# Performance work log

Measured on AMD Instinct MI355X. Metric: run time of the kernel, lower is better.

Reference implementation:

```python
import jax, jax.numpy as jnp
import numpy as np

H, D, J, T, IN = 8, 32, 22, 6, 256   # heads, head_dim, joint_num, time_len-2, input_dim
S = 3 * J                            # sequence axis of attention (66)
NEG = -9e15


def _domain_mask():
    m = np.ones((S, S), np.float32)
    m[0:J, 2 * J:3 * J] = 0.0
    m[2 * J:3 * J, 0:J] = 0.0
    return jnp.asarray(m)


def setup_inputs() -> dict:
    key = jax.random.key(0)
    ks = jax.random.split(key, 5)
    s = 0.02
    return {
        "x": jax.random.normal(ks[0], (512, T, S, IN), jnp.float32),
        "Wq": jax.random.normal(ks[1], (H * D, IN), jnp.float32) * s,
        "bq": jnp.zeros((H * D,), jnp.float32),
        "Wk": jax.random.normal(ks[2], (H * D, IN), jnp.float32) * s,
        "bk": jnp.zeros((H * D,), jnp.float32),
        "Wv": jax.random.normal(ks[3], (H * D, IN), jnp.float32) * s,
        "bv": jnp.zeros((H * D,), jnp.float32),
        "Wc": jax.random.normal(ks[4], (J, S), jnp.float32) * s,
        "bc": jnp.zeros((J,), jnp.float32),
    }


def reference(x, Wq, bq, Wk, bk, Wv, bv, Wc, bc):
    B = x.shape[0]
    mask = _domain_mask()

    def proj(W, b):
        # (B,T,S,IN) @ (IN,H*D) -> (B,T,S,H,D) -> (B,T,H,S,D)
        return (x @ W.T + b).reshape(B, T, S, H, D).transpose(0, 1, 3, 2, 4)

    q = proj(Wq, bq)
    k = proj(Wk, bk)
    v = jax.nn.relu(proj(Wv, bv))

    scores = jnp.einsum('bthqd,bthkd->bthqk', q, k) / jnp.sqrt(jnp.float32(D))
    scores = scores * mask
    # joint_num == 22 branch: threshold-based pruning against row max
    m = jnp.max(scores, axis=-1, keepdims=True)
    scores = jnp.where(jnp.abs(scores) <= m / 9.0, NEG, scores)
    attn = jax.nn.softmax(scores, axis=-1)

    out = jnp.einsum('bthqk,bthkd->bthqd', attn, v)          # (B,T,H,S,D)
    # cls Linear over the S axis: (B,T,H,D,S) -> (B,T,H,D,J), then back to (B,T,H,J,D)
    out = jnp.einsum('bthsd,js->bthjd', out, Wc) + bc[None, None, None, :, None]
    out = out.transpose(0, 1, 3, 2, 4)                        # (B,T,J,H,D)
    return out.reshape(B, T * J, H * D)
```

## Files before the change

kernel.cpp:

```cpp
#include <hip/hip_runtime.h>
#include <hip/hip_bf16.h>


constexpr int T  = 6;
constexpr int S  = 66;
constexpr int IN = 256;
constexpr int H  = 8;
constexpr int D  = 32;
constexpr int J  = 22;
constexpr float NEG = -9e15f;
constexpr float INV_SQRT_D = 0.17677669529663688110f;

#define XM2H_OFF 16384
#define XM2L_OFF 20480
#define W_OFF    24576
#define W_LO     12288
#define QH_OFF   0
#define QL_OFF   4752
#define KH_OFF   9504
#define KL_OFF   14256
#define VTH_OFF  28512
#define VTL_OFF  35168
#define INV_OFF  41824
#define AOT_OFF  42096
#define PH_OFF   0
#define PL_OFF   14256
#define P_STRIDE 216
#define WCH_OFF  28512
#define WCL_OFF  35168
#define SMEM_BYTES 49152

#define WSW_STRIDE 24576
#define WSWC_OFF   786432
#define WS_W       799744ull
#define XIMG_OFF   799744
#define XIMG_BT    65536
#define WS_FULL    (799744ull + 3072ull * 65536ull)

typedef float f32x4   __attribute__((ext_vector_type(4)));
typedef float f32x16  __attribute__((ext_vector_type(16)));
typedef short bf16x8  __attribute__((ext_vector_type(8)));
typedef short s4v     __attribute__((ext_vector_type(4)));

__device__ __forceinline__ unsigned cvtpk(float a, float b) {
    unsigned r;
    asm("v_cvt_pk_bf16_f32 %0, %1, %2" : "=v"(r) : "v"(a), "v"(b));
    return r;
}
__device__ __forceinline__ float bfh2f(unsigned short h) {
    return __uint_as_float(((unsigned)h) << 16);
}
__device__ __forceinline__ void split2(float a, float b, unsigned& hi, unsigned& lo) {
    unsigned h = cvtpk(a, b);
    float ra = a - __uint_as_float(h << 16);
    float rb = b - __uint_as_float(h & 0xffff0000u);
    lo = cvtpk(ra, rb);
    hi = h;
}
__device__ __forceinline__ bf16x8 ld_bf16x8_a8(const short* p) {
    s4v a = *(const s4v*)p;
    s4v b = *(const s4v*)(p + 4);
    return __builtin_shufflevector(a, b, 0, 1, 2, 3, 4, 5, 6, 7);
}
__device__ __forceinline__ void gload16(const void* g, void* l) {
    __builtin_amdgcn_global_load_lds(
        (const __attribute__((address_space(1))) unsigned*)g,
        (__attribute__((address_space(3))) unsigned*)l, 16, 0, 0);
}

__global__ __launch_bounds__(256)
void presplit_all(const float* __restrict__ Wq, const float* __restrict__ Wk,
                  const float* __restrict__ Wv, const float* __restrict__ Wc,
                  const float* __restrict__ x, unsigned char* __restrict__ ws)
{
    __shared__ __align__(16) unsigned char lds[16384];
    const int tid = threadIdx.x;
    if (blockIdx.x < 199) {
        int gid = blockIdx.x * 256 + tid;
        if (gid < 49152) {
            int img = gid / 1536, u = gid - img * 1536;
            int row = u >> 4, c = u & 15, k0 = c << 2;
            int mat = row >> 5, dd = row & 31;
            int chunk = img & 3, hh = img >> 2;
            const float* Wm = (mat == 0) ? Wq : (mat == 1) ? Wk : Wv;
            float4 v = *(const float4*)(Wm + (size_t)(hh * 32 + dd) * IN + chunk * 64 + c * 4);
            uint2 hi, lo;
            split2(v.x, v.y, hi.x, lo.x);
            split2(v.z, v.w, hi.y, lo.y);
            int tile  = (mat << 2) + (k0 >> 4);
            int lanei = dd + (((k0 >> 3) & 1) << 5);
            int byte  = (tile << 10) + (lanei << 4) + ((k0 & 7) << 1);
            unsigned char* base = ws + (size_t)img * WSW_STRIDE;
            *(uint2*)(base + byte)        = hi;
            *(uint2*)(base + W_LO + byte) = lo;
        } else if (gid < 49152 + 1664) {
            int g2  = gid - 49152;
            int row = g2 / 52, cu = g2 - row * 52;
            int c0  = 2 * cu;
            float a = (row < 22 && c0     < 66) ? Wc[row * 66 + c0]     : 0.f;
            float b = (row < 22 && c0 + 1 < 66) ? Wc[row * 66 + c0 + 1] : 0.f;
            unsigned hi, lo;
            split2(a, b, hi, lo);
            *(unsigned*)(ws + WSWC_OFF + row * 208 + 4 * cu)        = hi;
            *(unsigned*)(ws + WSWC_OFF + 6656 + row * 208 + 4 * cu) = lo;
        }
    } else {
        const int bid = blockIdx.x - 199;
        const int chunk = bid & 3;
        const int bt = bid >> 2;
        const float* xg = x + (size_t)bt * S * IN + chunk * 64;
        for (int u = tid; u < 1024; u += 256) {
            int s = u >> 4, c = u & 15;
            int rel = ((s << 7) + (c << 3)) ^ ((s & 7) << 4);
            float4 v = *(const float4*)(xg + (size_t)s * IN + c * 4);
            uint2 hi, lo;
            split2(v.x, v.y, hi.x, lo.x);
            split2(v.z, v.w, hi.y, lo.y);
            *(uint2*)(lds + rel)        = hi;
            *(uint2*)(lds + 8192 + rel) = lo;
        }
        __syncthreads();
        const int lane = tid & 63, wid = tid >> 6;
        unsigned char* img = ws + XIMG_OFF + (size_t)bt * XIMG_BT + chunk * 16384;
        for (int i = wid; i < 16; i += 4) {
            int comp = (i >= 8) ? 1 : 0;
            int ti = i - comp * 8;
            int mtile = ti >> 2, ks = ti & 3;
            int row = mtile * 32 + (lane & 31);
            int rel = ((row << 7) + (ks << 5) + ((lane >> 5) << 4)) ^ ((row & 7) << 4);
            uint4 v = *(const uint4*)(lds + comp * 8192 + rel);
            *(uint4*)(img + (i << 10) + (lane << 4)) = v;
        }
    }
}

template<int MODE>
__global__ __launch_bounds__(256, 3)
void mha_fused_kernel(const float* __restrict__ x,
                      const float* __restrict__ Wq, const float* __restrict__ bq,
                      const float* __restrict__ Wk, const float* __restrict__ bk,
                      const float* __restrict__ Wv, const float* __restrict__ bv,
                      const float* __restrict__ Wc, const float* __restrict__ bc,
                      const unsigned char* __restrict__ ws,
                      float* __restrict__ out)
{
    __shared__ __align__(16) unsigned char smem[SMEM_BYTES];

    const int tid = threadIdx.x;
    const int i0  = blockIdx.x;
    const int h   = (i0 >> 3) & 7;
    const int bt  = (i0 & 7) | ((i0 >> 6) << 3);

    const int wid  = tid >> 6;
    const int lane = tid & 63;
    const int l15  = lane & 15;
    const int quad = lane >> 4;

    for (int u = tid; u < 512; u += 256)
        *(uint4*)(smem + XM2H_OFF + u * 16) = (uint4){0u, 0u, 0u, 0u};

    const f32x16 zacc = {0.f,0.f,0.f,0.f,0.f,0.f,0.f,0.f,0.f,0.f,0.f,0.f,0.f,0.f,0.f,0.f};
    f32x16 accs[3] = {zacc, zacc, zacc};

    const float* xg0 = x + (size_t)bt * S * IN;
    for (int chunk = 0; chunk < 4; ++chunk) {
        __syncthreads();
        const float* xg = xg0 + chunk * 64;
        if constexpr (MODE == 2) {
            const unsigned char* ximg = ws + XIMG_OFF + (size_t)bt * XIMG_BT + chunk * 16384;
            const unsigned char* wimg = ws + (size_t)((h << 2) | chunk) * WSW_STRIDE;
            for (int i = wid; i < 16; i += 4)
                gload16(ximg + (i << 10) + (lane << 4), smem + (i << 10));
            for (int i = wid; i < 24; i += 4)
                gload16(wimg + (i << 10) + (lane << 4), smem + W_OFF + (i << 10));
            if (tid < 32) {
                int s = 64 + (tid >> 4), c = tid & 15;
                float4 v = *(const float4*)(xg + (size_t)s * IN + c * 4);
                uint2 hi, lo;
                split2(v.x, v.y, hi.x, lo.x);
                split2(v.z, v.w, hi.y, lo.y);
                int off = ((c >> 2) << 10) + (((s & 31) + (((c >> 1) & 1) << 5)) << 4)
                        + ((c & 1) << 3);
                *(uint2*)(smem + XM2H_OFF + off) = hi;
                *(uint2*)(smem + XM2L_OFF + off) = lo;
            }
        } else {
            if constexpr (MODE == 1) {
                const unsigned char* wimg = ws + (size_t)((h << 2) | chunk) * WSW_STRIDE;
                for (int i = wid; i < 24; i += 4)
                    gload16(wimg + (i << 10) + (lane << 4), smem + W_OFF + (i << 10));
            } else {
                for (int u = tid; u < 1536; u += 256) {
                    int row = u >> 4, c = u & 15, k0 = c << 2;
                    int mat = row >> 5, dd2 = row & 31;
                    const float* Wm = (mat == 0) ? Wq : (mat == 1) ? Wk : Wv;
                    float4 v = *(const float4*)(Wm + (size_t)(h * 32 + dd2) * IN + chunk * 64 + c * 4);
                    uint2 hi, lo;
                    split2(v.x, v.y, hi.x, lo.x);
                    split2(v.z, v.w, hi.y, lo.y);
                    int tile  = (mat << 2) + (k0 >> 4);
                    int lanei = dd2 + (((k0 >> 3) & 1) << 5);
                    int byte  = (tile << 10) + (lanei << 4) + ((k0 & 7) << 1);
                    *(uint2*)(smem + W_OFF + byte)        = hi;
                    *(uint2*)(smem + W_OFF + W_LO + byte) = lo;
                }
            }
            for (int u = tid; u < 1536; u += 256) {
                int s = u >> 4, c = u & 15, k0 = c << 2;
                if (s >= 66) continue;
                float4 v = *(const float4*)(xg + (size_t)s * IN + c * 4);
                uint2 hi, lo;
                split2(v.x, v.y, hi.x, lo.x);
                split2(v.z, v.w, hi.y, lo.y);
                int ks = k0 >> 4, khalf = (k0 >> 3) & 1, b = (k0 & 7) << 1;
                int off = (ks << 10) + (((s & 31) + (khalf << 5)) << 4) + b;
                if (s < 64) {
                    int base = (s >> 5) * 4096 + off;
                    *(uint2*)(smem + base)        = hi;
                    *(uint2*)(smem + base + 8192) = lo;
                } else {
                    *(uint2*)(smem + XM2H_OFF + off) = hi;
                    *(uint2*)(smem + XM2L_OFF + off) = lo;
                }
            }
        }
        __syncthreads();

        #pragma unroll
        for (int t = 0; t < 3; ++t) {
            int p = wid + 4 * t;
            if (p >= 9) break;
            int mtile = p / 3, mat = p - mtile * 3;
            const unsigned char *xaH, *xaL;
            if (mtile < 2) { xaH = smem + mtile * 4096 + (lane << 4); xaL = xaH + 8192; }
            else           { xaH = smem + XM2H_OFF + (lane << 4);     xaL = xaH + 4096; }
            const unsigned char* wbH = smem + W_OFF + mat * 4096 + (lane << 4);
            #pragma unroll
            for (int ks = 0; ks < 4; ++ks) {
                bf16x8 ah = *(const bf16x8*)(xaH + (ks << 10));
                bf16x8 al = *(const bf16x8*)(xaL + (ks << 10));
                bf16x8 bh = *(const bf16x8*)(wbH + (ks << 10));
                bf16x8 bl = *(const bf16x8*)(wbH + (ks << 10) + W_LO);
                accs[t] = __builtin_amdgcn_mfma_f32_32x32x16_bf16(ah, bh, accs[t], 0, 0, 0);
                accs[t] = __builtin_amdgcn_mfma_f32_32x32x16_bf16(ah, bl, accs[t], 0, 0, 0);
                accs[t] = __builtin_amdgcn_mfma_f32_32x32x16_bf16(al, bh, accs[t], 0, 0, 0);
            }
        }
    }
    __syncthreads();

    {
        short* qh = (short*)(smem + QH_OFF); short* ql = (short*)(smem + QL_OFF);
        short* kh = (short*)(smem + KH_OFF); short* kl = (short*)(smem + KL_OFF);
        const int dd = lane & 31;
        const int half = lane >> 5;
        #pragma unroll
        for (int t = 0; t < 3; ++t) {
            int p = wid + 4 * t;
            if (p >= 9) break;
            int mtile = p / 3, mat = p - mtile * 3;
            const float* bias_p = (mat == 0) ? bq : (mat == 1) ? bk : bv;
            float bias = bias_p[h * 32 + dd];
            if (mat < 2) {
                short* bh_ = (mat == 0) ? qh : kh;
                short* bl_ = (mat == 0) ? ql : kl;
                #pragma unroll
                for (int g = 0; g < 4; ++g) {
                    int sb2 = mtile * 32 + half * 4 + 8 * g;
                    uint2 hi, lo;
                    split2(accs[t][4*g+0] + bias, accs[t][4*g+1] + bias, hi.x, lo.x);
                    split2(accs[t][4*g+2] + bias, accs[t][4*g+3] + bias, hi.y, lo.y);
                    unsigned hs[4] = { hi.x & 0xffffu, hi.x >> 16, hi.y & 0xffffu, hi.y >> 16 };
                    unsigned ls[4] = { lo.x & 0xffffu, lo.x >> 16, lo.y & 0xffffu, lo.y >> 16 };
                    #pragma unroll
                    for (int r = 0; r < 4; ++r) {
                        int s = sb2 + r;
                        if (s < 66) {
                            bh_[s * 36 + dd] = (short)hs[r];
                            bl_[s * 36 + dd] = (short)ls[r];
                        }
                    }
                }
            } else {
                #pragma unroll
                for (int g = 0; g < 4; ++g) {
                    int sb2 = mtile * 32 + half * 4 + 8 * g;
                    float vv[4];
                    #pragma unroll
                    for (int r = 0; r < 4; ++r) {
                        int s = sb2 + r;
                        vv[r] = (s < 66) ? fmaxf(accs[t][4*g+r] + bias, 0.f) : 0.f;
                    }
                    uint2 ph, pl;
                    split2(vv[0], vv[1], ph.x, pl.x);
                    split2(vv[2], vv[3], ph.y, pl.y);
                    *(uint2*)(smem + VTH_OFF + dd * 208 + 2 * sb2) = ph;
                    *(uint2*)(smem + VTL_OFF + dd * 208 + 2 * sb2) = pl;
                }
            }
        }
    }
    __syncthreads();

    {
        const short* qh = (const short*)(smem + QH_OFF);
        const short* ql = (const short*)(smem + QL_OFF);
        const short* kh = (const short*)(smem + KH_OFF);
        const short* kl = (const short*)(smem + KL_OFF);

        auto qk_mfma = [&](int mq, f32x4* acc) {
            int boff = (mq * 16 + l15) * 36 + quad * 8;
            bf16x8 bh = ld_bf16x8_a8(qh + boff);
            bf16x8 bl = ld_bf16x8_a8(ql + boff);
            #pragma unroll
            for (int mk = 0; mk < 5; ++mk) {
                int aoff = (mk * 16 + l15) * 36 + quad * 8;
                bf16x8 ah = ld_bf16x8_a8(kh + aoff);
                bf16x8 al = ld_bf16x8_a8(kl + aoff);
                f32x4 a = (f32x4){0.f, 0.f, 0.f, 0.f};
                a = __builtin_amdgcn_mfma_f32_16x16x32_bf16(ah, bh, a, 0, 0, 0);
                a = __builtin_amdgcn_mfma_f32_16x16x32_bf16(ah, bl, a, 0, 0, 0);
                a = __builtin_amdgcn_mfma_f32_16x16x32_bf16(al, bh, a, 0, 0, 0);
                acc[mk] = a;
            }
        };

        f32x4 accA[5], accB[5];
        qk_mfma(wid, accA);
        if (wid == 3) qk_mfma(4, accB);
        __syncthreads();

        unsigned char* Ph = smem + PH_OFF;
        unsigned char* Pl = smem + PL_OFF;
        float* inv = (float*)(smem + INV_OFF);

        auto sm_store = [&](int mq, f32x4* acc) {
            const int q = mq * 16 + l15;
            float v[5][4];
            #pragma unroll
            for (int mk = 0; mk < 5; ++mk) {
                #pragma unroll
                for (int reg = 0; reg < 4; ++reg) {
                    int k = mk * 16 + quad * 4 + reg;
                    bool invalid = (k >= 66);
                    bool masked = (q < J && k >= 2 * J) || (q >= 2 * J && k < J);
                    float s = acc[mk][reg] * INV_SQRT_D;
                    v[mk][reg] = invalid ? -INFINITY : (masked ? 0.f : s);
                }
            }
            float mm = -INFINITY;
            #pragma unroll
            for (int mk = 0; mk < 5; ++mk)
                #pragma unroll
                for (int reg = 0; reg < 4; ++reg) mm = fmaxf(mm, v[mk][reg]);
            mm = fmaxf(mm, __shfl_xor(mm, 16));
            mm = fmaxf(mm, __shfl_xor(mm, 32));
            const float thr = mm / 9.0f;
            float rm = -INFINITY;
            #pragma unroll
            for (int mk = 0; mk < 5; ++mk) {
                #pragma unroll
                for (int reg = 0; reg < 4; ++reg) {
                    float sv = v[mk][reg];
                    float pr = (fabsf(sv) <= thr) ? NEG : sv;
                    v[mk][reg] = pr;
                    rm = fmaxf(rm, pr);
                }
            }
            rm = fmaxf(rm, __shfl_xor(rm, 16));
            rm = fmaxf(rm, __shfl_xor(rm, 32));
            float e[5][4], lsum = 0.f;
            #pragma unroll
            for (int mk = 0; mk < 5; ++mk) {
                #pragma unroll
                for (int reg = 0; reg < 4; ++reg) {
                    float ev = __expf(v[mk][reg] - rm);
                    e[mk][reg] = ev;
                    lsum += ev;
                }
            }
            lsum += __shfl_xor(lsum, 16);
            lsum += __shfl_xor(lsum, 32);
            if (q < 66) {
                #pragma unroll
                for (int mk = 0; mk < 5; ++mk) {
                    unsigned h0 = cvtpk(e[mk][0], e[mk][1]);
                    unsigned h1 = cvtpk(e[mk][2], e[mk][3]);
                    uint2 hi = {h0, h1}, lo;
                    lo.x = cvtpk(e[mk][0] - bfh2f((unsigned short)h0),
                                 e[mk][1] - bfh2f((unsigned short)(h0 >> 16)));
                    lo.y = cvtpk(e[mk][2] - bfh2f((unsigned short)h1),
                                 e[mk][3] - bfh2f((unsigned short)(h1 >> 16)));
                    int kb = (mk * 16 + quad * 4) * 2;
                    *(uint2*)(Ph + q * P_STRIDE + kb) = hi;
                    *(uint2*)(Pl + q * P_STRIDE + kb) = lo;
                }
                if (quad == 0) inv[q] = 1.0f / lsum;
            }
        };

        sm_store(wid, accA);
        if (wid == 3) sm_store(4, accB);

        for (int u = tid; u < 528; u += 256) {
            int comp = u >= 264 ? 1 : 0, rem = u - comp * 264;
            int row = rem >> 2, slot = rem & 3;
            *(uint2*)(smem + (comp ? PL_OFF : PH_OFF) + row * P_STRIDE + 160 + slot * 8)
                = (uint2){0u, 0u};
        }
    }
    __syncthreads();

    {
        const short* Ph = (const short*)(smem + PH_OFF);
        const short* Pl = (const short*)(smem + PL_OFF);
        const short* vh = (const short*)(smem + VTH_OFF);
        const short* vl = (const short*)(smem + VTL_OFF);
        const float* inv = (const float*)(smem + INV_OFF);
        for (int t = 0; t < 3; ++t) {
            int tt = wid + 4 * t;
            if (tt >= 10) break;
            int mq = tt >> 1, nd = tt & 1;
            f32x4 acc = (f32x4){0.f, 0.f, 0.f, 0.f};
            #pragma unroll
            for (int ks = 0; ks < 3; ++ks) {
                bf16x8 a   = ld_bf16x8_a8(Ph + (mq * 16 + l15) * 108 + ks * 32 + quad * 8);
                bf16x8 al8 = ld_bf16x8_a8(Pl + (mq * 16 + l15) * 108 + ks * 32 + quad * 8);
                bf16x8 b   = *(const bf16x8*)(vh + (nd * 16 + l15) * 104 + ks * 32 + quad * 8);
                bf16x8 bl8 = *(const bf16x8*)(vl + (nd * 16 + l15) * 104 + ks * 32 + quad * 8);
                acc = __builtin_amdgcn_mfma_f32_16x16x32_bf16(a, b, acc, 0, 0, 0);
                acc = __builtin_amdgcn_mfma_f32_16x16x32_bf16(al8, b, acc, 0, 0, 0);
                acc = __builtin_amdgcn_mfma_f32_16x16x32_bf16(a, bl8, acc, 0, 0, 0);
            }
            int dd = nd * 16 + l15, sbase = mq * 16 + quad * 4;
            float o[4];
            #pragma unroll
            for (int reg = 0; reg < 4; ++reg) {
                int qs = sbase + reg;
                o[reg] = (qs < 66) ? acc[reg] * inv[qs] : 0.f;
            }
            uint2 pk;
            pk.x = cvtpk(o[0], o[1]);
            pk.y = cvtpk(o[2], o[3]);
            *(uint2*)(smem + AOT_OFF + dd * 208 + 2 * sbase) = pk;
        }
        for (int u = tid; u < 384; u += 256) {
            int row = u / 12, kcol = 80 + 2 * (u % 12);
            *(unsigned*)(smem + AOT_OFF + row * 208 + 2 * kcol) = 0u;
        }
    }
    __syncthreads();

    if constexpr (MODE >= 1) {
        const unsigned char* wc = ws + WSWC_OFF;
        for (int i = wid; i < 13; i += 4)
            gload16(wc + (i << 10) + (lane << 4), smem + WCH_OFF + (i << 10));
    } else {
        for (int u = tid; u < 726; u += 256) {
            int row = u / 33, cp = u - row * 33;
            float2 w = *(const float2*)(Wc + row * 66 + 2 * cp);
            unsigned hi, lo;
            split2(w.x, w.y, hi, lo);
            *(unsigned*)(smem + WCH_OFF + row * 208 + 4 * cp) = hi;
            *(unsigned*)(smem + WCL_OFF + row * 208 + 4 * cp) = lo;
        }
        for (int u = tid; u < 836; u += 256) {
            int comp = u >= 418 ? 1 : 0, rem = comp ? u - 418 : u;
            int row = rem / 19, kcol = 66 + 2 * (rem % 19);
            *(unsigned*)(smem + (comp ? WCL_OFF : WCH_OFF) + row * 208 + 2 * kcol) = 0u;
        }
    }
    __syncthreads();

    {
        const short* Wch = (const short*)(smem + WCH_OFF);
        const short* Wcl = (const short*)(smem + WCL_OFF);
        const short* aoT = (const short*)(smem + AOT_OFF);
        int mj = wid >> 1, nd = wid & 1;
        f32x4 acc = (f32x4){0.f, 0.f, 0.f, 0.f};
        #pragma unroll
        for (int ks = 0; ks < 3; ++ks) {
            bf16x8 a   = *(const bf16x8*)(Wch + (mj * 16 + l15) * 104 + ks * 32 + quad * 8);
            bf16x8 al8 = *(const bf16x8*)(Wcl + (mj * 16 + l15) * 104 + ks * 32 + quad * 8);
            bf16x8 b   = *(const bf16x8*)(aoT + (nd * 16 + l15) * 104 + ks * 32 + quad * 8);
            acc = __builtin_amdgcn_mfma_f32_16x16x32_bf16(a, b, acc, 0, 0, 0);
            acc = __builtin_amdgcn_mfma_f32_16x16x32_bf16(al8, b, acc, 0, 0, 0);
        }
        int dd = nd * 16 + l15;
        #pragma unroll
        for (int reg = 0; reg < 4; ++reg) {
            int j = mj * 16 + quad * 4 + reg;
            if (j < 22) {
                size_t o = (size_t)(bt * J + j) * (H * D) + h * 32 + dd;
                out[o] = acc[reg] + bc[j];
            }
        }
    }
}

extern "C" void kernel_launch(void* const* d_in, const int* in_sizes, int n_in,
                              void* d_out, int out_size, void* d_ws, size_t ws_size,
                              hipStream_t stream) {
    const float* x  = (const float*)d_in[0];
    const float* Wq = (const float*)d_in[1];
    const float* bq = (const float*)d_in[2];
    const float* Wk = (const float*)d_in[3];
    const float* bk = (const float*)d_in[4];
    const float* Wv = (const float*)d_in[5];
    const float* bv = (const float*)d_in[6];
    const float* Wc = (const float*)d_in[7];
    const float* bc = (const float*)d_in[8];
    float* out = (float*)d_out;

    const int B = 512;
    dim3 grid(B * T * H), block(256);
    if (d_ws != nullptr && ws_size >= WS_FULL) {
        hipLaunchKernelGGL(presplit_all, dim3(199 + 12288), dim3(256), 0, stream,
                           Wq, Wk, Wv, Wc, x, (unsigned char*)d_ws);
        hipLaunchKernelGGL((mha_fused_kernel<2>), grid, block, 0, stream,
                           x, Wq, bq, Wk, bk, Wv, bv, Wc, bc,
                           (const unsigned char*)d_ws, out);
    } else if (d_ws != nullptr && ws_size >= WS_W) {
        hipLaunchKernelGGL(presplit_all, dim3(199), dim3(256), 0, stream,
                           Wq, Wk, Wv, Wc, x, (unsigned char*)d_ws);
        hipLaunchKernelGGL((mha_fused_kernel<1>), grid, block, 0, stream,
                           x, Wq, bq, Wk, bk, Wv, bv, Wc, bc,
                           (const unsigned char*)d_ws, out);
    } else {
        hipLaunchKernelGGL((mha_fused_kernel<0>), grid, block, 0, stream,
                           x, Wq, bq, Wk, bk, Wv, bv, Wc, bc,
                           (const unsigned char*)nullptr, out);
    }
}
```

Before: 881.5 us.

## Shrink LDS footprint by streaming weights from global and peeling key tail

```diff
diff --git a/kernel.cpp b/kernel.cpp
--- a/kernel.cpp
+++ b/kernel.cpp
@@ -13,29 +13,29 @@
 
 #define XM2H_OFF 16384
 #define XM2L_OFF 20480
-#define W_OFF    24576
-#define W_LO     12288
 #define QH_OFF   0
 #define QL_OFF   4752
 #define KH_OFF   9504
 #define KL_OFF   14256
-#define VTH_OFF  28512
-#define VTL_OFF  35168
-#define INV_OFF  41824
-#define AOT_OFF  42096
 #define PH_OFF   0
-#define PL_OFF   14256
-#define P_STRIDE 216
-#define WCH_OFF  28512
-#define WCL_OFF  35168
-#define SMEM_BYTES 49152
+#define PL_OFF   8976
+#define P64_OFF  17952
+#define INV_OFF  18480
+#define VTH_OFF  19008
+#define VTL_OFF  23360
+#define V64_OFF  27712
+#define AOT_OFF  27968
+#define AO64_OFF 32320
+#define SMEM_BYTES 32576
+#define PV_ROW   68
 
 #define WSW_STRIDE 24576
+#define W_LO       12288
 #define WSWC_OFF   786432
-#define WS_W       799744ull
-#define XIMG_OFF   799744
+#define WS_W       794624ull
+#define XIMG_OFF   794624
 #define XIMG_BT    65536
-#define WS_FULL    (799744ull + 3072ull * 65536ull)
+#define WS_FULL    (794624ull + 3072ull * 65536ull)
 
 typedef float f32x4   __attribute__((ext_vector_type(4)));
 typedef float f32x16  __attribute__((ext_vector_type(16)));
@@ -93,16 +93,19 @@
             unsigned char* base = ws + (size_t)img * WSW_STRIDE;
             *(uint2*)(base + byte)        = hi;
             *(uint2*)(base + W_LO + byte) = lo;
-        } else if (gid < 49152 + 1664) {
+        } else if (gid < 49152 + 1024) {
             int g2  = gid - 49152;
-            int row = g2 / 52, cu = g2 - row * 52;
-            int c0  = 2 * cu;
-            float a = (row < 22 && c0     < 66) ? Wc[row * 66 + c0]     : 0.f;
-            float b = (row < 22 && c0 + 1 < 66) ? Wc[row * 66 + c0 + 1] : 0.f;
+            int row = g2 >> 5, cu = g2 & 31;
+            int k0  = 2 * cu;
+            float a = (row < 22) ? Wc[row * 66 + k0]     : 0.f;
+            float b = (row < 22) ? Wc[row * 66 + k0 + 1] : 0.f;
             unsigned hi, lo;
             split2(a, b, hi, lo);
-            *(unsigned*)(ws + WSWC_OFF + row * 208 + 4 * cu)        = hi;
-            *(unsigned*)(ws + WSWC_OFF + 6656 + row * 208 + 4 * cu) = lo;
+            int tile = (row >> 4) * 2 + (k0 >> 5);
+            int byte = (tile << 10) + (((row & 15) + 16 * ((k0 >> 3) & 3)) << 4)
+                     + ((k0 & 7) << 1);
+            *(unsigned*)(ws + WSWC_OFF + byte)        = hi;
+            *(unsigned*)(ws + WSWC_OFF + 4096 + byte) = lo;
         }
     } else {
         const int bid = blockIdx.x - 199;
@@ -135,7 +138,7 @@
 }
 
 template<int MODE>
-__global__ __launch_bounds__(256, 3)
+__global__ __launch_bounds__(256, 5)
 void mha_fused_kernel(const float* __restrict__ x,
                       const float* __restrict__ Wq, const float* __restrict__ bq,
                       const float* __restrict__ Wk, const float* __restrict__ bk,
@@ -166,13 +169,11 @@
     for (int chunk = 0; chunk < 4; ++chunk) {
         __syncthreads();
         const float* xg = xg0 + chunk * 64;
+        const unsigned char* wimg = ws + (size_t)((h << 2) | chunk) * WSW_STRIDE;
         if constexpr (MODE == 2) {
             const unsigned char* ximg = ws + XIMG_OFF + (size_t)bt * XIMG_BT + chunk * 16384;
-            const unsigned char* wimg = ws + (size_t)((h << 2) | chunk) * WSW_STRIDE;
             for (int i = wid; i < 16; i += 4)
                 gload16(ximg + (i << 10) + (lane << 4), smem + (i << 10));
-            for (int i = wid; i < 24; i += 4)
-                gload16(wimg + (i << 10) + (lane << 4), smem + W_OFF + (i << 10));
             if (tid < 32) {
                 int s = 64 + (tid >> 4), c = tid & 15;
                 float4 v = *(const float4*)(xg + (size_t)s * IN + c * 4);
@@ -185,26 +186,6 @@
                 *(uint2*)(smem + XM2L_OFF + off) = lo;
             }
         } else {
-            if constexpr (MODE == 1) {
-                const unsigned char* wimg = ws + (size_t)((h << 2) | chunk) * WSW_STRIDE;
-                for (int i = wid; i < 24; i += 4)
-                    gload16(wimg + (i << 10) + (lane << 4), smem + W_OFF + (i << 10));
-            } else {
-                for (int u = tid; u < 1536; u += 256) {
-                    int row = u >> 4, c = u & 15, k0 = c << 2;
-                    int mat = row >> 5, dd2 = row & 31;
-                    const float* Wm = (mat == 0) ? Wq : (mat == 1) ? Wk : Wv;
-                    float4 v = *(const float4*)(Wm + (size_t)(h * 32 + dd2) * IN + chunk * 64 + c * 4);
-                    uint2 hi, lo;
-                    split2(v.x, v.y, hi.x, lo.x);
-                    split2(v.z, v.w, hi.y, lo.y);
-                    int tile  = (mat << 2) + (k0 >> 4);
-                    int lanei = dd2 + (((k0 >> 3) & 1) << 5);
-                    int byte  = (tile << 10) + (lanei << 4) + ((k0 & 7) << 1);
-                    *(uint2*)(smem + W_OFF + byte)        = hi;
-                    *(uint2*)(smem + W_OFF + W_LO + byte) = lo;
-                }
-            }
             for (int u = tid; u < 1536; u += 256) {
                 int s = u >> 4, c = u & 15, k0 = c << 2;
                 if (s >= 66) continue;
@@ -234,13 +215,28 @@
             const unsigned char *xaH, *xaL;
             if (mtile < 2) { xaH = smem + mtile * 4096 + (lane << 4); xaL = xaH + 8192; }
             else           { xaH = smem + XM2H_OFF + (lane << 4);     xaL = xaH + 4096; }
-            const unsigned char* wbH = smem + W_OFF + mat * 4096 + (lane << 4);
             #pragma unroll
             for (int ks = 0; ks < 4; ++ks) {
+                bf16x8 bh, bl;
+                if constexpr (MODE >= 1) {
+                    const unsigned char* wt = wimg + (((mat * 4 + ks)) << 10) + (lane << 4);
+                    bh = *(const bf16x8*)(wt);
+                    bl = *(const bf16x8*)(wt + W_LO);
+                } else {
+                    const float* Wm = (mat == 0) ? Wq : (mat == 1) ? Wk : Wv;
+                    const float* wrow = Wm + (size_t)(h * 32 + (lane & 31)) * IN
+                                      + chunk * 64 + ks * 16 + (lane >> 5) * 8;
+                    float4 w0 = *(const float4*)wrow, w1 = *(const float4*)(wrow + 4);
+                    uint4 uh, ul;
+                    split2(w0.x, w0.y, uh.x, ul.x);
+                    split2(w0.z, w0.w, uh.y, ul.y);
+                    split2(w1.x, w1.y, uh.z, ul.z);
+                    split2(w1.z, w1.w, uh.w, ul.w);
+                    bh = *(bf16x8*)&uh;
+                    bl = *(bf16x8*)&ul;
+                }
                 bf16x8 ah = *(const bf16x8*)(xaH + (ks << 10));
                 bf16x8 al = *(const bf16x8*)(xaL + (ks << 10));
-                bf16x8 bh = *(const bf16x8*)(wbH + (ks << 10));
-                bf16x8 bl = *(const bf16x8*)(wbH + (ks << 10) + W_LO);
                 accs[t] = __builtin_amdgcn_mfma_f32_32x32x16_bf16(ah, bh, accs[t], 0, 0, 0);
                 accs[t] = __builtin_amdgcn_mfma_f32_32x32x16_bf16(ah, bl, accs[t], 0, 0, 0);
                 accs[t] = __builtin_amdgcn_mfma_f32_32x32x16_bf16(al, bh, accs[t], 0, 0, 0);
@@ -291,11 +287,15 @@
                         int s = sb2 + r;
                         vv[r] = (s < 66) ? fmaxf(accs[t][4*g+r] + bias, 0.f) : 0.f;
                     }
-                    uint2 ph, pl;
-                    split2(vv[0], vv[1], ph.x, pl.x);
-                    split2(vv[2], vv[3], ph.y, pl.y);
-                    *(uint2*)(smem + VTH_OFF + dd * 208 + 2 * sb2) = ph;
-                    *(uint2*)(smem + VTL_OFF + dd * 208 + 2 * sb2) = pl;
+                    if (sb2 < 64) {
+                        uint2 ph, pl;
+                        split2(vv[0], vv[1], ph.x, pl.x);
+                        split2(vv[2], vv[3], ph.y, pl.y);
+                        *(uint2*)(smem + VTH_OFF + dd * 136 + 2 * sb2) = ph;
+                        *(uint2*)(smem + VTL_OFF + dd * 136 + 2 * sb2) = pl;
+                    } else if (sb2 == 64) {
+                        *(float2*)(smem + V64_OFF + dd * 8) = (float2){vv[0], vv[1]};
+                    }
                 }
             }
         }
@@ -383,7 +383,7 @@
             lsum += __shfl_xor(lsum, 32);
             if (q < 66) {
                 #pragma unroll
-                for (int mk = 0; mk < 5; ++mk) {
+                for (int mk = 0; mk < 4; ++mk) {
                     unsigned h0 = cvtpk(e[mk][0], e[mk][1]);
                     unsigned h1 = cvtpk(e[mk][2], e[mk][3]);
                     uint2 hi = {h0, h1}, lo;
@@ -391,23 +391,19 @@
                                  e[mk][1] - bfh2f((unsigned short)(h0 >> 16)));
                     lo.y = cvtpk(e[mk][2] - bfh2f((unsigned short)h1),
                                  e[mk][3] - bfh2f((unsigned short)(h1 >> 16)));
-                    int kb = (mk * 16 + quad * 4) * 2;
-                    *(uint2*)(Ph + q * P_STRIDE + kb) = hi;
-                    *(uint2*)(Pl + q * P_STRIDE + kb) = lo;
-                }
-                if (quad == 0) inv[q] = 1.0f / lsum;
+                    int kb = mk * 32 + quad * 8;
+                    *(uint2*)(Ph + q * 136 + kb) = hi;
+                    *(uint2*)(Pl + q * 136 + kb) = lo;
+                }
+                if (quad == 0) {
+                    *(float2*)(smem + P64_OFF + q * 8) = (float2){e[4][0], e[4][1]};
+                    inv[q] = 1.0f / lsum;
+                }
             }
         };
 
         sm_store(wid, accA);
         if (wid == 3) sm_store(4, accB);
-
-        for (int u = tid; u < 528; u += 256) {
-            int comp = u >= 264 ? 1 : 0, rem = u - comp * 264;
-            int row = rem >> 2, slot = rem & 3;
-            *(uint2*)(smem + (comp ? PL_OFF : PH_OFF) + row * P_STRIDE + 160 + slot * 8)
-                = (uint2){0u, 0u};
-        }
     }
     __syncthreads();
 
@@ -421,78 +417,82 @@
             int tt = wid + 4 * t;
             if (tt >= 10) break;
             int mq = tt >> 1, nd = tt & 1;
+            int arow = (mq * 16 + l15) * PV_ROW;
+            int brow = (nd * 16 + l15) * PV_ROW;
             f32x4 acc = (f32x4){0.f, 0.f, 0.f, 0.f};
             #pragma unroll
-            for (int ks = 0; ks < 3; ++ks) {
-                bf16x8 a   = ld_bf16x8_a8(Ph + (mq * 16 + l15) * 108 + ks * 32 + quad * 8);
-                bf16x8 al8 = ld_bf16x8_a8(Pl + (mq * 16 + l15) * 108 + ks * 32 + quad * 8);
-                bf16x8 b   = *(const bf16x8*)(vh + (nd * 16 + l15) * 104 + ks * 32 + quad * 8);
-                bf16x8 bl8 = *(const bf16x8*)(vl + (nd * 16 + l15) * 104 + ks * 32 + quad * 8);
+            for (int ks = 0; ks < 2; ++ks) {
+                bf16x8 a   = ld_bf16x8_a8(Ph + arow + ks * 32 + quad * 8);
+                bf16x8 al8 = ld_bf16x8_a8(Pl + arow + ks * 32 + quad * 8);
+                bf16x8 b   = ld_bf16x8_a8(vh + brow + ks * 32 + quad * 8);
+                bf16x8 bl8 = ld_bf16x8_a8(vl + brow + ks * 32 + quad * 8);
                 acc = __builtin_amdgcn_mfma_f32_16x16x32_bf16(a, b, acc, 0, 0, 0);
                 acc = __builtin_amdgcn_mfma_f32_16x16x32_bf16(al8, b, acc, 0, 0, 0);
                 acc = __builtin_amdgcn_mfma_f32_16x16x32_bf16(a, bl8, acc, 0, 0, 0);
             }
             int dd = nd * 16 + l15, sbase = mq * 16 + quad * 4;
+            float2 vdd = *(const float2*)(smem + V64_OFF + dd * 8);
             float o[4];
             #pragma unroll
             for (int reg = 0; reg < 4; ++reg) {
                 int qs = sbase + reg;
-                o[reg] = (qs < 66) ? acc[reg] * inv[qs] : 0.f;
-            }
-            uint2 pk;
-            pk.x = cvtpk(o[0], o[1]);
-            pk.y = cvtpk(o[2], o[3]);
-            *(uint2*)(smem + AOT_OFF + dd * 208 + 2 * sbase) = pk;
-        }
-        for (int u = tid; u < 384; u += 256) {
-            int row = u / 12, kcol = 80 + 2 * (u % 12);
-            *(unsigned*)(smem + AOT_OFF + row * 208 + 2 * kcol) = 0u;
+                float2 p2 = *(const float2*)(smem + P64_OFF + qs * 8);
+                float tv = acc[reg] + p2.x * vdd.x + p2.y * vdd.y;
+                o[reg] = (qs < 66) ? tv * inv[qs] : 0.f;
+            }
+            if (sbase < 64) {
+                uint2 pk;
+                pk.x = cvtpk(o[0], o[1]);
+                pk.y = cvtpk(o[2], o[3]);
+                *(uint2*)(smem + AOT_OFF + dd * 136 + 2 * sbase) = pk;
+            } else if (quad == 0) {
+                *(float2*)(smem + AO64_OFF + dd * 8) = (float2){o[0], o[1]};
+            }
         }
     }
     __syncthreads();
 
-    if constexpr (MODE >= 1) {
-        const unsigned char* wc = ws + WSWC_OFF;
-        for (int i = wid; i < 13; i += 4)
-            gload16(wc + (i << 10) + (lane << 4), smem + WCH_OFF + (i << 10));
-    } else {
-        for (int u = tid; u < 726; u += 256) {
-            int row = u / 33, cp = u - row * 33;
-            float2 w = *(const float2*)(Wc + row * 66 + 2 * cp);
-            unsigned hi, lo;
-            split2(w.x, w.y, hi, lo);
-            *(unsigned*)(smem + WCH_OFF + row * 208 + 4 * cp) = hi;
-            *(unsigned*)(smem + WCL_OFF + row * 208 + 4 * cp) = lo;
-        }
-        for (int u = tid; u < 836; u += 256) {
-            int comp = u >= 418 ? 1 : 0, rem = comp ? u - 418 : u;
-            int row = rem / 19, kcol = 66 + 2 * (rem % 19);
-            *(unsigned*)(smem + (comp ? WCL_OFF : WCH_OFF) + row * 208 + 2 * kcol) = 0u;
-        }
-    }
-    __syncthreads();
-
     {
-        const short* Wch = (const short*)(smem + WCH_OFF);
-        const short* Wcl = (const short*)(smem + WCL_OFF);
         const short* aoT = (const short*)(smem + AOT_OFF);
         int mj = wid >> 1, nd = wid & 1;
         f32x4 acc = (f32x4){0.f, 0.f, 0.f, 0.f};
         #pragma unroll
-        for (int ks = 0; ks < 3; ++ks) {
-            bf16x8 a   = *(const bf16x8*)(Wch + (mj * 16 + l15) * 104 + ks * 32 + quad * 8);
-            bf16x8 al8 = *(const bf16x8*)(Wcl + (mj * 16 + l15) * 104 + ks * 32 + quad * 8);
-            bf16x8 b   = *(const bf16x8*)(aoT + (nd * 16 + l15) * 104 + ks * 32 + quad * 8);
+        for (int ks = 0; ks < 2; ++ks) {
+            bf16x8 a, al8;
+            if constexpr (MODE >= 1) {
+                const unsigned char* wt = ws + WSWC_OFF + ((mj * 2 + ks) << 10) + (lane << 4);
+                a   = *(const bf16x8*)(wt);
+                al8 = *(const bf16x8*)(wt + 4096);
+            } else {
+                float4 w0 = {0.f,0.f,0.f,0.f}, w1 = w0;
+                int jr = mj * 16 + l15;
+                if (jr < 22) {
+                    const float* p = Wc + jr * 66 + ks * 32 + quad * 8;
+                    w0 = *(const float4*)p;
+                    w1 = *(const float4*)(p + 4);
+                }
+                uint4 uh, ul;
+                split2(w0.x, w0.y, uh.x, ul.x);
+                split2(w0.z, w0.w, uh.y, ul.y);
+                split2(w1.x, w1.y, uh.z, ul.z);
+                split2(w1.z, w1.w, uh.w, ul.w);
+                a   = *(bf16x8*)&uh;
+                al8 = *(bf16x8*)&ul;
+            }
+            bf16x8 b = ld_bf16x8_a8(aoT + (nd * 16 + l15) * PV_ROW + ks * 32 + quad * 8);
             acc = __builtin_amdgcn_mfma_f32_16x16x32_bf16(a, b, acc, 0, 0, 0);
             acc = __builtin_amdgcn_mfma_f32_16x16x32_bf16(al8, b, acc, 0, 0, 0);
         }
         int dd = nd * 16 + l15;
+        float2 ao2 = *(const float2*)(smem + AO64_OFF + dd * 8);
         #pragma unroll
         for (int reg = 0; reg < 4; ++reg) {
             int j = mj * 16 + quad * 4 + reg;
             if (j < 22) {
+                float w64a = Wc[j * 66 + 64], w64b = Wc[j * 66 + 65];
+                float r = acc[reg] + w64a * ao2.x + w64b * ao2.y + bc[j];
                 size_t o = (size_t)(bt * J + j) * (H * D) + h * 32 + dd;
-                out[o] = acc[reg] + bc[j];
+                out[o] = r;
             }
         }
     }
```

New measurement: 806.0 us. 8.6% less time.
